# Optimization experiments

Hardware: AMD Instinct MI355X
Metric: run time of the kernel (lower is better)

The kernel has to match this reference:

```python
import jax, jax.numpy as jnp
import numpy as np


def setup_inputs() -> dict:
    key = jax.random.key(0)
    ks = jax.random.split(key, 5)
    n, raw, d, h = 1024, 128, 128, 256
    s = lambda fan: 1.0 / np.sqrt(fan)
    return {
        "x": jax.random.normal(ks[0], (n, raw), jnp.float32),
        "W_enc": jax.random.normal(ks[1], (raw, d), jnp.float32) * s(raw),
        "b_enc": jnp.zeros((d,), jnp.float32),
        "W1": jax.random.normal(ks[2], (2 * d, h), jnp.float32) * s(2 * d),
        "b1": jnp.zeros((h,), jnp.float32),
        "W2": jax.random.normal(ks[3], (h, 1), jnp.float32) * s(h),
        "b2": jnp.zeros((1,), jnp.float32),
    }


def reference(x, W_enc, b_enc, W1, b1, W2, b2):
    # pathVAE.encode stand-in: linear projection to latent mean
    z = x @ W_enc + b_enc                      # [n, d]
    n, d = z.shape
    # Original builds feat[i, j] = concat(z[j], z[i]) of shape [n*n, 2d],
    # then Linear(2d->h). Split W1 so the quadratic concat is never built:
    # h[i, j] = z[j] @ W1[:d] + z[i] @ W1[d:] + b1
    A = z @ W1[:d]                             # acts on the "a" (j) half
    B = z @ W1[d:]                             # acts on the "b" (i) half
    hmat = A[None, :, :] + B[:, None, :] + b1  # [n, n, h]
    hmat = jax.nn.selu(hmat)
    o = hmat @ W2 + b2                         # [n, n, 1]
    o = jax.nn.hard_sigmoid(o)                 # relu6(x+3)/6, same as torch
    return o.reshape(n, n)
```

## Files before the change

kernel.cpp:

```cpp
#include <hip/hip_runtime.h>
#include <math.h>


#define LOG2E       1.4426950408889634f
#define SELU_AS     1.7580993408473766f
#define S_OVER_L2E  0.7282921587620419f

typedef float v2f __attribute__((ext_vector_type(2)));
typedef _Float16 v2h __attribute__((ext_vector_type(2)));
typedef unsigned int u32;

__global__ __launch_bounds__(256) void prep_kernel(
    const float* __restrict__ x, const float* __restrict__ W_enc,
    const float* __restrict__ b_enc, const float* __restrict__ W1,
    const float* __restrict__ b1, const float* __restrict__ W2,
    const float* __restrict__ b2, u32* __restrict__ PAa,
    u32* __restrict__ PAe, u32* __restrict__ PBb, u32* __restrict__ PBe,
    u32* __restrict__ W2m, u32* __restrict__ W2e, float* __restrict__ basep)
{
    __shared__ float zs[512];
    int t = threadIdx.x, b = blockIdx.x;
    if (b < 256) {
        int r0 = b << 2;
        int r = t >> 6;
        int dd = (t & 63) << 1;
        const float* xr = x + (size_t)(r0 + r) * 128;
        v2f z = { b_enc[dd], b_enc[dd + 1] };
#pragma unroll 8
        for (int dl = 0; dl < 128; ++dl) {
            float xv = xr[dl];
            v2f xx = { xv, xv };
            v2f wv = *(const v2f*)(W_enc + (size_t)dl * 128 + dd);
            z = __builtin_elementwise_fma(xx, wv, z);
        }
        zs[r * 128 + dd] = z.x;
        zs[r * 128 + dd + 1] = z.y;
        __syncthreads();

        int c = t;
        float b1c = b1[c];
        float accA0 = 0.f, accA1 = 0.f, accA2 = 0.f, accA3 = 0.f;
        float accB0 = b1c, accB1 = b1c, accB2 = b1c, accB3 = b1c;
        const float* w1a = W1 + c;
        const float* w1b = W1 + 128 * 256 + c;
#pragma unroll 4
        for (int dl = 0; dl < 128; ++dl) {
            float wa = w1a[(size_t)dl * 256];
            float wb = w1b[(size_t)dl * 256];
            float z0 = zs[dl], z1 = zs[128 + dl], z2 = zs[256 + dl], z3 = zs[384 + dl];
            accA0 = fmaf(z0, wa, accA0); accB0 = fmaf(z0, wb, accB0);
            accA1 = fmaf(z1, wa, accA1); accB1 = fmaf(z1, wb, accB1);
            accA2 = fmaf(z2, wa, accA2); accB2 = fmaf(z2, wb, accB2);
            accA3 = fmaf(z3, wa, accA3); accB3 = fmaf(z3, wb, accB3);
        }
        float ar[4] = { accA0 * LOG2E, accA1 * LOG2E, accA2 * LOG2E, accA3 * LOG2E };
        float br[4] = { accB0 * LOG2E, accB1 * LOG2E, accB2 * LOG2E, accB3 * LOG2E };
        u32 pa[4], pe[4], pb[4], pf[4];
        bool odd = (c & 1);
#pragma unroll
        for (int r2 = 0; r2 < 4; ++r2) {
            float er = __builtin_amdgcn_exp2f(ar[r2]);
            float fr = __builtin_amdgcn_exp2f(br[r2]);
            float aN = __shfl_xor(ar[r2], 1);
            float eN = __shfl_xor(er, 1);
            float bN = __shfl_xor(br[r2], 1);
            float fN = __shfl_xor(fr, 1);
            pa[r2] = __builtin_bit_cast(u32, __builtin_amdgcn_cvt_pkrtz(ar[r2], aN));
            pe[r2] = __builtin_bit_cast(u32, __builtin_amdgcn_cvt_pkrtz(er, eN));
            pb[r2] = __builtin_bit_cast(u32, __builtin_amdgcn_cvt_pkrtz(bN, br[r2]));
            pf[r2] = __builtin_bit_cast(u32, __builtin_amdgcn_cvt_pkrtz(fN, fr));
        }
        size_t o = (size_t)(c >> 1) * 1024 + r0;
        if (!odd) {
            *(uint4*)(PAa + o) = make_uint4(pa[0], pa[1], pa[2], pa[3]);
            *(uint4*)(PAe + o) = make_uint4(pe[0], pe[1], pe[2], pe[3]);
        } else {
            *(uint4*)(PBb + o) = make_uint4(pb[0], pb[1], pb[2], pb[3]);
            *(uint4*)(PBe + o) = make_uint4(pf[0], pf[1], pf[2], pf[3]);
        }
    } else {
        if (t < 128) {
            float w0 = W2[2 * t], w1 = W2[2 * t + 1];
            W2m[t] = __builtin_bit_cast(u32,
                __builtin_amdgcn_cvt_pkrtz(S_OVER_L2E * w0, S_OVER_L2E * w1));
            W2e[t] = __builtin_bit_cast(u32,
                __builtin_amdgcn_cvt_pkrtz(SELU_AS * w0, SELU_AS * w1));
        }
        if (t < 64) {
            float s = W2[t] + W2[t + 64] + W2[t + 128] + W2[t + 192];
#pragma unroll
            for (int o = 32; o > 0; o >>= 1) s += __shfl_down(s, o);
            if (t == 0) basep[0] = fmaf(-SELU_AS, s, b2[0]);
        }
    }
}

__global__ __launch_bounds__(1024, 4) void pair_kernel(
    const u32* __restrict__ PAa, const u32* __restrict__ PAe,
    const u32* __restrict__ PBb, const u32* __restrict__ PBe,
    const u32* __restrict__ W2m, const u32* __restrict__ W2e,
    const float* __restrict__ basep, float* __restrict__ out)
{
    __shared__ __align__(16) u32 S[16384];

    int t = threadIdx.x;
    int q = t >> 8;
    int tq = t & 255;
    int bj64 = blockIdx.x << 6, bi64 = blockIdx.y << 6;
    int tj4 = (tq & 15) << 2, ti4 = (tq >> 4) << 2;

    u32* Q  = S + (q << 12);
    u32* Aa = Q;
    u32* Ae = Q + 1024;
    u32* Bb = Q + 2048;
    u32* Be = Q + 3072;

    float acc[4][4];
#pragma unroll
    for (int i = 0; i < 4; ++i)
#pragma unroll
        for (int j = 0; j < 4; ++j) acc[i][j] = 0.f;

    const v2h hzero = { (_Float16)0.f, (_Float16)0.f };
    const v2h hone  = { (_Float16)1.f, (_Float16)1.f };

    int s_k2l = tq >> 4;
    int s_jq  = (tq & 15) << 2;

    for (int sc = 0; sc < 2; ++sc) {
        int k2base = (q << 5) + (sc << 4);
        if (sc) __syncthreads();
        {
            size_t go = (size_t)(k2base + s_k2l) * 1024;
            *(uint4*)&Aa[tq << 2] = *(const uint4*)(PAa + go + bj64 + s_jq);
            *(uint4*)&Ae[tq << 2] = *(const uint4*)(PAe + go + bj64 + s_jq);
            *(uint4*)&Bb[tq << 2] = *(const uint4*)(PBb + go + bi64 + s_jq);
            *(uint4*)&Be[tq << 2] = *(const uint4*)(PBe + go + bi64 + s_jq);
        }
        __syncthreads();

        const u32* Wm = W2m + k2base;
        const u32* We = W2e + k2base;
#pragma unroll 4
        for (int k2 = 0; k2 < 16; ++k2) {
            v2h w2m = __builtin_bit_cast(v2h, Wm[k2]);
            v2h w2e = __builtin_bit_cast(v2h, We[k2]);
            uint4 qa = *(const uint4*)&Aa[(k2 << 6) + tj4];
            uint4 qe = *(const uint4*)&Ae[(k2 << 6) + tj4];
            uint4 qb = *(const uint4*)&Bb[(k2 << 6) + ti4];
            uint4 qf = *(const uint4*)&Be[(k2 << 6) + ti4];
            v2h a[4] = { __builtin_bit_cast(v2h, qa.x), __builtin_bit_cast(v2h, qa.y),
                         __builtin_bit_cast(v2h, qa.z), __builtin_bit_cast(v2h, qa.w) };
            v2h e[4] = { __builtin_bit_cast(v2h, qe.x), __builtin_bit_cast(v2h, qe.y),
                         __builtin_bit_cast(v2h, qe.z), __builtin_bit_cast(v2h, qe.w) };
            v2h bb[4] = { __builtin_bit_cast(v2h, qb.x), __builtin_bit_cast(v2h, qb.y),
                          __builtin_bit_cast(v2h, qb.z), __builtin_bit_cast(v2h, qb.w) };
            v2h ff[4] = { __builtin_bit_cast(v2h, qf.x), __builtin_bit_cast(v2h, qf.y),
                          __builtin_bit_cast(v2h, qf.z), __builtin_bit_cast(v2h, qf.w) };
#pragma unroll
            for (int i = 0; i < 4; ++i) {
#pragma unroll
                for (int j = 0; j < 4; ++j) {
                    v2h t2 = a[j] + bb[i];
                    v2h p2 = e[j] * ff[i];
                    v2h m2 = __builtin_elementwise_max(t2, hzero);
                    v2h n2 = __builtin_elementwise_min(p2, hone);
                    acc[i][j] = __builtin_amdgcn_fdot2(m2, w2m, acc[i][j], false);
                    acc[i][j] = __builtin_amdgcn_fdot2(n2, w2e, acc[i][j], false);
                }
            }
        }
    }

    __syncthreads();
    if (q != 0) {
        float4* dst = (float4*)Q;
#pragma unroll
        for (int i = 0; i < 4; ++i) {
            float4 v;
            v.x = acc[i][0]; v.y = acc[i][1]; v.z = acc[i][2]; v.w = acc[i][3];
            dst[(tq << 2) + i] = v;
        }
    }
    __syncthreads();
    if (q == 0) {
        float base = basep[0];
        const float4* Q1 = (const float4*)(S + 4096);
        const float4* Q2 = (const float4*)(S + 8192);
        const float4* Q3 = (const float4*)(S + 12288);
#pragma unroll
        for (int i = 0; i < 4; ++i) {
            float4 p1 = Q1[(tq << 2) + i];
            float4 p2 = Q2[(tq << 2) + i];
            float4 p3 = Q3[(tq << 2) + i];
            float v0 = acc[i][0] + p1.x + p2.x + p3.x + base;
            float v1 = acc[i][1] + p1.y + p2.y + p3.y + base;
            float v2 = acc[i][2] + p1.z + p2.z + p3.z + base;
            float v3 = acc[i][3] + p1.w + p2.w + p3.w + base;
            float4 o;
            o.x = __saturatef(v0 * (1.0f / 6.0f) + 0.5f);
            o.y = __saturatef(v1 * (1.0f / 6.0f) + 0.5f);
            o.z = __saturatef(v2 * (1.0f / 6.0f) + 0.5f);
            o.w = __saturatef(v3 * (1.0f / 6.0f) + 0.5f);
            *(float4*)(out + (size_t)(bi64 + ti4 + i) * 1024 + bj64 + tj4) = o;
        }
    }
}

extern "C" void kernel_launch(void* const* d_in, const int* in_sizes, int n_in,
                              void* d_out, int out_size, void* d_ws, size_t ws_size,
                              hipStream_t stream) {
    const float* x     = (const float*)d_in[0];
    const float* W_enc = (const float*)d_in[1];
    const float* b_enc = (const float*)d_in[2];
    const float* W1    = (const float*)d_in[3];
    const float* b1    = (const float*)d_in[4];
    const float* W2    = (const float*)d_in[5];
    const float* b2    = (const float*)d_in[6];
    float* out = (float*)d_out;

    u32* ws = (u32*)d_ws;
    const int PLANE = 128 * 1024;
    u32* PAa = ws;
    u32* PAe = ws + PLANE;
    u32* PBb = ws + 2 * PLANE;
    u32* PBe = ws + 3 * PLANE;
    u32* W2m = ws + 4 * PLANE;
    u32* W2e = ws + 4 * PLANE + 128;
    float* basep = (float*)(ws + 4 * PLANE + 256);

    prep_kernel<<<257, 256, 0, stream>>>(x, W_enc, b_enc, W1, b1, W2, b2,
                                         PAa, PAe, PBb, PBe, W2m, W2e, basep);
    pair_kernel<<<dim3(16, 16), 1024, 0, stream>>>(PAa, PAe, PBb, PBe,
                                                   W2m, W2e, basep, out);
}
```

Measured before the change: 112.2 us.

## Use 8x8 register tiles per thread with per-wave k-split and tree reduction

The pair kernel drops from 1024 to 512 threads per block. Each thread now computes an 8x8 output tile instead of 4x4, and each of the 8 waves owns a private slice of the hidden dimension. Waves stage their own LDS tiles without block-wide barriers, relying only on an lgkmcnt wait, which cuts the LDS reads per FLOP and removes sync overhead in the main loop. The per-wave partial sums are combined with a three-level tree reduction through shared memory. The cost is more accumulator registers per thread and less parallelism per block.

```diff
diff --git a/kernel.cpp b/kernel.cpp
--- a/kernel.cpp
+++ b/kernel.cpp
@@ -95,7 +95,7 @@
     }
 }
 
-__global__ __launch_bounds__(1024, 4) void pair_kernel(
+__global__ __launch_bounds__(512, 2) void pair_kernel(
     const u32* __restrict__ PAa, const u32* __restrict__ PAe,
     const u32* __restrict__ PBb, const u32* __restrict__ PBe,
     const u32* __restrict__ W2m, const u32* __restrict__ W2e,
@@ -104,65 +104,79 @@
     __shared__ __align__(16) u32 S[16384];
 
     int t = threadIdx.x;
-    int q = t >> 8;
-    int tq = t & 255;
+    int w = t >> 6;
+    int lt = t & 63;
     int bj64 = blockIdx.x << 6, bi64 = blockIdx.y << 6;
-    int tj4 = (tq & 15) << 2, ti4 = (tq >> 4) << 2;
-
-    u32* Q  = S + (q << 12);
+    int jb = (lt & 7) << 3;
+    int ib = (lt >> 3) << 3;
+
+    u32* Q  = S + (w << 11);
     u32* Aa = Q;
-    u32* Ae = Q + 1024;
-    u32* Bb = Q + 2048;
-    u32* Be = Q + 3072;
-
-    float acc[4][4];
-#pragma unroll
-    for (int i = 0; i < 4; ++i)
-#pragma unroll
-        for (int j = 0; j < 4; ++j) acc[i][j] = 0.f;
+    u32* Ae = Q + 512;
+    u32* Bb = Q + 1024;
+    u32* Be = Q + 1536;
+
+    float acc[8][8];
+#pragma unroll
+    for (int i = 0; i < 8; ++i)
+#pragma unroll
+        for (int j = 0; j < 8; ++j) acc[i][j] = 0.f;
 
     const v2h hzero = { (_Float16)0.f, (_Float16)0.f };
     const v2h hone  = { (_Float16)1.f, (_Float16)1.f };
 
-    int s_k2l = tq >> 4;
-    int s_jq  = (tq & 15) << 2;
-
     for (int sc = 0; sc < 2; ++sc) {
-        int k2base = (q << 5) + (sc << 4);
-        if (sc) __syncthreads();
-        {
-            size_t go = (size_t)(k2base + s_k2l) * 1024;
-            *(uint4*)&Aa[tq << 2] = *(const uint4*)(PAa + go + bj64 + s_jq);
-            *(uint4*)&Ae[tq << 2] = *(const uint4*)(PAe + go + bj64 + s_jq);
-            *(uint4*)&Bb[tq << 2] = *(const uint4*)(PBb + go + bi64 + s_jq);
-            *(uint4*)&Be[tq << 2] = *(const uint4*)(PBe + go + bi64 + s_jq);
-        }
-        __syncthreads();
+        int k2base = (w << 4) + (sc << 3);
+        asm volatile("" ::: "memory");
+#pragma unroll
+        for (int p = 0; p < 2; ++p) {
+            int idx = (p << 6) + lt;
+            int row = idx >> 4;
+            int col = (idx & 15) << 2;
+            size_t go = (size_t)(k2base + row) * 1024;
+            *(uint4*)&Aa[idx << 2] = *(const uint4*)(PAa + go + bj64 + col);
+            *(uint4*)&Ae[idx << 2] = *(const uint4*)(PAe + go + bj64 + col);
+            *(uint4*)&Bb[idx << 2] = *(const uint4*)(PBb + go + bi64 + col);
+            *(uint4*)&Be[idx << 2] = *(const uint4*)(PBe + go + bi64 + col);
+        }
+        asm volatile("s_waitcnt lgkmcnt(0)" ::: "memory");
 
         const u32* Wm = W2m + k2base;
         const u32* We = W2e + k2base;
 #pragma unroll 4
-        for (int k2 = 0; k2 < 16; ++k2) {
+        for (int k2 = 0; k2 < 8; ++k2) {
             v2h w2m = __builtin_bit_cast(v2h, Wm[k2]);
             v2h w2e = __builtin_bit_cast(v2h, We[k2]);
-            uint4 qa = *(const uint4*)&Aa[(k2 << 6) + tj4];
-            uint4 qe = *(const uint4*)&Ae[(k2 << 6) + tj4];
-            uint4 qb = *(const uint4*)&Bb[(k2 << 6) + ti4];
-            uint4 qf = *(const uint4*)&Be[(k2 << 6) + ti4];
-            v2h a[4] = { __builtin_bit_cast(v2h, qa.x), __builtin_bit_cast(v2h, qa.y),
-                         __builtin_bit_cast(v2h, qa.z), __builtin_bit_cast(v2h, qa.w) };
-            v2h e[4] = { __builtin_bit_cast(v2h, qe.x), __builtin_bit_cast(v2h, qe.y),
-                         __builtin_bit_cast(v2h, qe.z), __builtin_bit_cast(v2h, qe.w) };
-            v2h bb[4] = { __builtin_bit_cast(v2h, qb.x), __builtin_bit_cast(v2h, qb.y),
-                          __builtin_bit_cast(v2h, qb.z), __builtin_bit_cast(v2h, qb.w) };
-            v2h ff[4] = { __builtin_bit_cast(v2h, qf.x), __builtin_bit_cast(v2h, qf.y),
-                          __builtin_bit_cast(v2h, qf.z), __builtin_bit_cast(v2h, qf.w) };
-#pragma unroll
-            for (int i = 0; i < 4; ++i) {
-#pragma unroll
-                for (int j = 0; j < 4; ++j) {
-                    v2h t2 = a[j] + bb[i];
-                    v2h p2 = e[j] * ff[i];
+            uint4 qa0 = *(const uint4*)&Aa[(k2 << 6) + jb];
+            uint4 qa1 = *(const uint4*)&Aa[(k2 << 6) + jb + 4];
+            uint4 qe0 = *(const uint4*)&Ae[(k2 << 6) + jb];
+            uint4 qe1 = *(const uint4*)&Ae[(k2 << 6) + jb + 4];
+            uint4 qb0 = *(const uint4*)&Bb[(k2 << 6) + ib];
+            uint4 qb1 = *(const uint4*)&Bb[(k2 << 6) + ib + 4];
+            uint4 qf0 = *(const uint4*)&Be[(k2 << 6) + ib];
+            uint4 qf1 = *(const uint4*)&Be[(k2 << 6) + ib + 4];
+            v2h A[8] = { __builtin_bit_cast(v2h, qa0.x), __builtin_bit_cast(v2h, qa0.y),
+                         __builtin_bit_cast(v2h, qa0.z), __builtin_bit_cast(v2h, qa0.w),
+                         __builtin_bit_cast(v2h, qa1.x), __builtin_bit_cast(v2h, qa1.y),
+                         __builtin_bit_cast(v2h, qa1.z), __builtin_bit_cast(v2h, qa1.w) };
+            v2h E[8] = { __builtin_bit_cast(v2h, qe0.x), __builtin_bit_cast(v2h, qe0.y),
+                         __builtin_bit_cast(v2h, qe0.z), __builtin_bit_cast(v2h, qe0.w),
+                         __builtin_bit_cast(v2h, qe1.x), __builtin_bit_cast(v2h, qe1.y),
+                         __builtin_bit_cast(v2h, qe1.z), __builtin_bit_cast(v2h, qe1.w) };
+            v2h B[8] = { __builtin_bit_cast(v2h, qb0.x), __builtin_bit_cast(v2h, qb0.y),
+                         __builtin_bit_cast(v2h, qb0.z), __builtin_bit_cast(v2h, qb0.w),
+                         __builtin_bit_cast(v2h, qb1.x), __builtin_bit_cast(v2h, qb1.y),
+                         __builtin_bit_cast(v2h, qb1.z), __builtin_bit_cast(v2h, qb1.w) };
+            v2h F[8] = { __builtin_bit_cast(v2h, qf0.x), __builtin_bit_cast(v2h, qf0.y),
+                         __builtin_bit_cast(v2h, qf0.z), __builtin_bit_cast(v2h, qf0.w),
+                         __builtin_bit_cast(v2h, qf1.x), __builtin_bit_cast(v2h, qf1.y),
+                         __builtin_bit_cast(v2h, qf1.z), __builtin_bit_cast(v2h, qf1.w) };
+#pragma unroll
+            for (int i = 0; i < 8; ++i) {
+#pragma unroll
+                for (int j = 0; j < 8; ++j) {
+                    v2h t2 = A[j] + B[i];
+                    v2h p2 = E[j] * F[i];
                     v2h m2 = __builtin_elementwise_max(t2, hzero);
                     v2h n2 = __builtin_elementwise_min(p2, hone);
                     acc[i][j] = __builtin_amdgcn_fdot2(m2, w2m, acc[i][j], false);
@@ -172,39 +186,60 @@
         }
     }
 
-    __syncthreads();
-    if (q != 0) {
-        float4* dst = (float4*)Q;
-#pragma unroll
-        for (int i = 0; i < 4; ++i) {
-            float4 v;
-            v.x = acc[i][0]; v.y = acc[i][1]; v.z = acc[i][2]; v.w = acc[i][3];
-            dst[(tq << 2) + i] = v;
+    float4* buf = (float4*)S;
+#define STORE_ACC(REG) {                                                  \
+        float4* r_ = buf + ((REG) << 10);                                 \
+        _Pragma("unroll")                                                 \
+        for (int i = 0; i < 8; ++i) {                                     \
+            float4 lo = { acc[i][0], acc[i][1], acc[i][2], acc[i][3] };   \
+            float4 hi = { acc[i][4], acc[i][5], acc[i][6], acc[i][7] };   \
+            r_[((i << 1) + 0) * 64 + lt] = lo;                            \
+            r_[((i << 1) + 1) * 64 + lt] = hi;                            \
+        } }
+#define ADD_ACC(REG) {                                                    \
+        float4* r_ = buf + ((REG) << 10);                                 \
+        _Pragma("unroll")                                                 \
+        for (int i = 0; i < 8; ++i) {                                     \
+            float4 lo = r_[((i << 1) + 0) * 64 + lt];                     \
+            float4 hi = r_[((i << 1) + 1) * 64 + lt];                     \
+            acc[i][0] += lo.x; acc[i][1] += lo.y;                         \
+            acc[i][2] += lo.z; acc[i][3] += lo.w;                         \
+            acc[i][4] += hi.x; acc[i][5] += hi.y;                         \
+            acc[i][6] += hi.z; acc[i][7] += hi.w;                         \
+        } }
+
+    __syncthreads();
+    if (w >= 4) STORE_ACC(w - 4);
+    __syncthreads();
+    if (w < 4) ADD_ACC(w);
+    __syncthreads();
+    if (w == 2 || w == 3) STORE_ACC(w - 2);
+    __syncthreads();
+    if (w < 2) ADD_ACC(w);
+    __syncthreads();
+    if (w == 1) STORE_ACC(0);
+    __syncthreads();
+    if (w == 0) {
+        ADD_ACC(0);
+        float base = basep[0];
+#pragma unroll
+        for (int i = 0; i < 8; ++i) {
+            float4 o0, o1;
+            o0.x = __saturatef((acc[i][0] + base) * (1.0f / 6.0f) + 0.5f);
+            o0.y = __saturatef((acc[i][1] + base) * (1.0f / 6.0f) + 0.5f);
+            o0.z = __saturatef((acc[i][2] + base) * (1.0f / 6.0f) + 0.5f);
+            o0.w = __saturatef((acc[i][3] + base) * (1.0f / 6.0f) + 0.5f);
+            o1.x = __saturatef((acc[i][4] + base) * (1.0f / 6.0f) + 0.5f);
+            o1.y = __saturatef((acc[i][5] + base) * (1.0f / 6.0f) + 0.5f);
+            o1.z = __saturatef((acc[i][6] + base) * (1.0f / 6.0f) + 0.5f);
+            o1.w = __saturatef((acc[i][7] + base) * (1.0f / 6.0f) + 0.5f);
+            size_t orow = (size_t)(bi64 + ib + i) * 1024 + bj64 + jb;
+            *(float4*)(out + orow) = o0;
+            *(float4*)(out + orow + 4) = o1;
         }
     }
-    __syncthreads();
-    if (q == 0) {
-        float base = basep[0];
-        const float4* Q1 = (const float4*)(S + 4096);
-        const float4* Q2 = (const float4*)(S + 8192);
-        const float4* Q3 = (const float4*)(S + 12288);
-#pragma unroll
-        for (int i = 0; i < 4; ++i) {
-            float4 p1 = Q1[(tq << 2) + i];
-            float4 p2 = Q2[(tq << 2) + i];
-            float4 p3 = Q3[(tq << 2) + i];
-            float v0 = acc[i][0] + p1.x + p2.x + p3.x + base;
-            float v1 = acc[i][1] + p1.y + p2.y + p3.y + base;
-            float v2 = acc[i][2] + p1.z + p2.z + p3.z + base;
-            float v3 = acc[i][3] + p1.w + p2.w + p3.w + base;
-            float4 o;
-            o.x = __saturatef(v0 * (1.0f / 6.0f) + 0.5f);
-            o.y = __saturatef(v1 * (1.0f / 6.0f) + 0.5f);
-            o.z = __saturatef(v2 * (1.0f / 6.0f) + 0.5f);
-            o.w = __saturatef(v3 * (1.0f / 6.0f) + 0.5f);
-            *(float4*)(out + (size_t)(bi64 + ti4 + i) * 1024 + bj64 + tj4) = o;
-        }
-    }
+#undef STORE_ACC
+#undef ADD_ACC
 }
 
 extern "C" void kernel_launch(void* const* d_in, const int* in_sizes, int n_in,
@@ -231,6 +266,6 @@
 
     prep_kernel<<<257, 256, 0, stream>>>(x, W_enc, b_enc, W1, b1, W2, b2,
                                          PAa, PAe, PBb, PBe, W2m, W2e, basep);
-    pair_kernel<<<dim3(16, 16), 1024, 0, stream>>>(PAa, PAe, PBb, PBe,
-                                                   W2m, W2e, basep, out);
+    pair_kernel<<<dim3(16, 16), 512, 0, stream>>>(PAa, PAe, PBb, PBe,
+                                                  W2m, W2e, basep, out);
 }
```

Result: no change. 111.8 us (-0.3%).
